# Performance work log

Measured on AMD Instinct MI355X. Metric: run time of the kernel, lower is better.

The kernel has to match this reference:

```python
import jax, jax.numpy as jnp
import numpy as np

BN_EPS = 1e-5
N_NODES = 131072
C_IN = 32
C_OUT = 32
K = 27  # 3x3x3 kernel taps


def setup_inputs() -> dict:
    key = jax.random.key(0)
    k1, k2, k3 = jax.random.split(key, 3)
    data_in = jax.random.normal(k1, (1, C_IN, N_NODES, 1), dtype=jnp.float32)
    neigh = jax.random.randint(k2, (N_NODES, K), 0, N_NODES, dtype=jnp.int32)
    weight = jax.random.normal(k3, (K * C_IN, C_OUT), dtype=jnp.float32) * (1.0 / np.sqrt(K * C_IN))
    gamma = jnp.ones((C_OUT,), dtype=jnp.float32)
    beta = jnp.zeros((C_OUT,), dtype=jnp.float32)
    return {"data_in": data_in, "neigh": neigh, "weight": weight, "gamma": gamma, "beta": beta}


def reference(data_in, neigh, weight, gamma, beta):
    # data_in: [1, C_in, N, 1] -> node-major features [N, C_in]
    x = jnp.transpose(data_in[0, :, :, 0])  # [N, C_in]
    # Octree sparse conv: gather 27-neighborhood per node, then matmul.
    g = x[neigh]                              # [N, K, C_in] irregular gather
    g = g.reshape(g.shape[0], K * C_IN)       # [N, K*C_in]
    out = g @ weight                          # [N, C_out]
    # BatchNorm2d over [1, C_out, N, 1]: per-channel stats over the N nodes (training mode, biased var)
    mean = jnp.mean(out, axis=0)
    var = jnp.mean(jnp.square(out - mean), axis=0)
    out = (out - mean) * jax.lax.rsqrt(var + BN_EPS) * gamma + beta
    # ReLU
    out = jnp.maximum(out, 0.0)
    # back to O-CNN layout [1, C_out, N, 1]
    return jnp.transpose(out)[None, :, :, None]
```

## Files before the change

kernel.cpp:

```cpp
#include <hip/hip_runtime.h>

#define N_NODES 131072
#define C_IN 32
#define C_OUT 32
#define KTAPS 27
#define BN_EPS 1e-5f

typedef __bf16 bf16x8 __attribute__((ext_vector_type(8)));
typedef float  f32x4  __attribute__((ext_vector_type(4)));


static __device__ __forceinline__ unsigned short f2bf(float f) {
    unsigned int u = __float_as_uint(f);
    unsigned int r = (u + 0x7FFFu + ((u >> 16) & 1u)) >> 16;
    return (unsigned short)r;
}

__global__ __launch_bounds__(256) void k_prep_x(const float* __restrict__ in,
                                                unsigned short* __restrict__ xb) {
    const int n = blockIdx.x * 256 + threadIdx.x;
    unsigned short v[C_IN];
#pragma unroll
    for (int c = 0; c < C_IN; ++c) v[c] = f2bf(in[(size_t)c * N_NODES + n]);
    uint4* dst = reinterpret_cast<uint4*>(xb + (size_t)n * C_IN);
#pragma unroll
    for (int q = 0; q < 4; ++q) {
        uint4 pk;
        pk.x = (unsigned)v[q * 8 + 0] | ((unsigned)v[q * 8 + 1] << 16);
        pk.y = (unsigned)v[q * 8 + 2] | ((unsigned)v[q * 8 + 3] << 16);
        pk.z = (unsigned)v[q * 8 + 4] | ((unsigned)v[q * 8 + 5] << 16);
        pk.w = (unsigned)v[q * 8 + 6] | ((unsigned)v[q * 8 + 7] << 16);
        dst[q] = pk;
    }
}

__global__ __launch_bounds__(256) void k_prep_w(const float* __restrict__ w,
                                                unsigned short* __restrict__ wlay) {
    const int g = blockIdx.x * 256 + threadIdx.x;
    if (g >= KTAPS * 2 * 64) return;
    const int k = g >> 7;
    const int rem = g & 127;
    const int h = rem >> 6;
    const int l = rem & 63;
    unsigned short v[8];
#pragma unroll
    for (int j = 0; j < 8; ++j) {
        const int c  = ((l >> 4) << 3) + j;
        const int co = (h << 4) + (l & 15);
        v[j] = f2bf(w[(size_t)(k * C_IN + c) * C_OUT + co]);
    }
    uint4 pk;
    pk.x = (unsigned)v[0] | ((unsigned)v[1] << 16);
    pk.y = (unsigned)v[2] | ((unsigned)v[3] << 16);
    pk.z = (unsigned)v[4] | ((unsigned)v[5] << 16);
    pk.w = (unsigned)v[6] | ((unsigned)v[7] << 16);
    *reinterpret_cast<uint4*>(wlay + (size_t)g * 8) = pk;
}

__global__ __launch_bounds__(256) void k_conv_mfma(const unsigned short* __restrict__ xb,
                                                   const int* __restrict__ neigh,
                                                   const unsigned short* __restrict__ wlay,
                                                   float* __restrict__ out) {
    const int wid  = threadIdx.x >> 6;
    const int lane = threadIdx.x & 63;
    const int lr   = lane & 15;
    const int lg   = lane >> 4;
    const int nb   = (blockIdx.x * 4 + wid) * 16;

    const int* nrow = neigh + (size_t)(nb + lr) * KTAPS;
    int nidx[KTAPS];
#pragma unroll
    for (int k = 0; k < KTAPS; ++k) nidx[k] = nrow[k];

    f32x4 acc0 = {0.f, 0.f, 0.f, 0.f};
    f32x4 acc1 = {0.f, 0.f, 0.f, 0.f};

#pragma unroll
    for (int k = 0; k < KTAPS; ++k) {
        const bf16x8 xf = *reinterpret_cast<const bf16x8*>(xb + (size_t)nidx[k] * C_IN + lg * 8);
        const bf16x8 w0 = *reinterpret_cast<const bf16x8*>(wlay + ((size_t)(k * 2 + 0) * 64 + lane) * 8);
        const bf16x8 w1 = *reinterpret_cast<const bf16x8*>(wlay + ((size_t)(k * 2 + 1) * 64 + lane) * 8);
        acc0 = __builtin_amdgcn_mfma_f32_16x16x32_bf16(w0, xf, acc0, 0, 0, 0);
        acc1 = __builtin_amdgcn_mfma_f32_16x16x32_bf16(w1, xf, acc1, 0, 0, 0);
    }

#pragma unroll
    for (int r = 0; r < 4; ++r) {
        out[(size_t)(lg * 4 + r) * N_NODES + nb + lr]        = acc0[r];
        out[(size_t)(16 + lg * 4 + r) * N_NODES + nb + lr]   = acc1[r];
    }
}

__global__ __launch_bounds__(256) void k_stats(const float* __restrict__ out,
                                               float* __restrict__ sums) {
    const int c     = blockIdx.x >> 3;
    const int chunk = blockIdx.x & 7;
    const float4* base = reinterpret_cast<const float4*>(out + (size_t)c * N_NODES + chunk * (N_NODES / 8));
    float s = 0.f, s2 = 0.f;
    for (int i = threadIdx.x; i < N_NODES / 8 / 4; i += 256) {
        float4 v = base[i];
        s  += v.x + v.y + v.z + v.w;
        s2 += v.x * v.x + v.y * v.y + v.z * v.z + v.w * v.w;
    }
#pragma unroll
    for (int off = 32; off >= 1; off >>= 1) {
        s  += __shfl_xor(s,  off);
        s2 += __shfl_xor(s2, off);
    }
    __shared__ float ls[8];
    const int wid = threadIdx.x >> 6;
    if ((threadIdx.x & 63) == 0) { ls[wid * 2] = s; ls[wid * 2 + 1] = s2; }
    __syncthreads();
    if (threadIdx.x == 0) {
        float ts  = ls[0] + ls[2] + ls[4] + ls[6];
        float ts2 = ls[1] + ls[3] + ls[5] + ls[7];
        atomicAdd(&sums[c], ts);
        atomicAdd(&sums[C_OUT + c], ts2);
    }
}

__global__ __launch_bounds__(256) void k_bnrelu(float* __restrict__ out,
                                                const float* __restrict__ sums,
                                                const float* __restrict__ gamma,
                                                const float* __restrict__ beta) {
    const size_t gid = (size_t)blockIdx.x * 256 + threadIdx.x;
    const int co = (int)(gid / (N_NODES / 4));
    const float inv_n = 1.0f / (float)N_NODES;
    const float mean = sums[co] * inv_n;
    const float var  = sums[C_OUT + co] * inv_n - mean * mean;
    const float scale = rsqrtf(var + BN_EPS) * gamma[co];
    const float bias  = beta[co] - mean * scale;

    float4* p = reinterpret_cast<float4*>(out);
    float4 v = p[gid];
    v.x = fmaxf(fmaf(v.x, scale, bias), 0.0f);
    v.y = fmaxf(fmaf(v.y, scale, bias), 0.0f);
    v.z = fmaxf(fmaf(v.z, scale, bias), 0.0f);
    v.w = fmaxf(fmaf(v.w, scale, bias), 0.0f);
    p[gid] = v;
}

extern "C" void kernel_launch(void* const* d_in, const int* in_sizes, int n_in,
                              void* d_out, int out_size, void* d_ws, size_t ws_size,
                              hipStream_t stream) {
    const float* data_in = (const float*)d_in[0];
    const int*   neigh   = (const int*)d_in[1];
    const float* weight  = (const float*)d_in[2];
    const float* gamma   = (const float*)d_in[3];
    const float* beta    = (const float*)d_in[4];
    float* out = (float*)d_out;

    unsigned short* xb   = (unsigned short*)d_ws;
    unsigned short* wlay = xb + (size_t)N_NODES * C_IN;
    float* sums = (float*)(wlay + (size_t)KTAPS * 2 * 64 * 8);

    hipMemsetAsync(sums, 0, 2 * C_OUT * sizeof(float), stream);
    k_prep_x<<<N_NODES / 256, 256, 0, stream>>>(data_in, xb);
    k_prep_w<<<(KTAPS * 2 * 64 + 255) / 256, 256, 0, stream>>>(weight, wlay);
    k_conv_mfma<<<N_NODES / 64, 256, 0, stream>>>(xb, neigh, wlay, out);
    k_stats<<<C_OUT * 8, 256, 0, stream>>>(out, sums);
    k_bnrelu<<<(N_NODES * C_OUT / 4) / 256, 256, 0, stream>>>(out, sums, gamma, beta);
}
```

Before: 82.52 us.

## Partition gather by source range in passes, stage weights in LDS, merge prep kernels

The conv kernel now makes three passes over the node index range. Each pass only gathers neighbors whose index falls in the current third and redirects the rest to a zero padding row, to improve cache locality of the irregular gather. Weights are staged in shared memory, each wave processes 64 nodes instead of 16, and the two prep kernels are merged into one launch. The cost is triple the MFMA and index-load work, plus fewer blocks and waves to hide gather latency.

Result: slower. 125.0 us (+51.5%).

```diff
diff --git a/kernel.cpp b/kernel.cpp
--- a/kernel.cpp
+++ b/kernel.cpp
@@ -5,6 +5,7 @@
 #define C_OUT 32
 #define KTAPS 27
 #define BN_EPS 1e-5f
+#define NPASS 3
 
 typedef __bf16 bf16x8 __attribute__((ext_vector_type(8)));
 typedef float  f32x4  __attribute__((ext_vector_type(4)));
@@ -16,8 +17,10 @@
     return (unsigned short)r;
 }
 
-__global__ __launch_bounds__(256) void k_prep_x(const float* __restrict__ in,
-                                                unsigned short* __restrict__ xb) {
+__global__ __launch_bounds__(256) void k_prep(const float* __restrict__ in,
+                                              const float* __restrict__ w,
+                                              unsigned short* __restrict__ xb,
+                                              unsigned short* __restrict__ wlay) {
     const int n = blockIdx.x * 256 + threadIdx.x;
     unsigned short v[C_IN];
 #pragma unroll
@@ -32,63 +35,84 @@
         pk.w = (unsigned)v[q * 8 + 6] | ((unsigned)v[q * 8 + 7] << 16);
         dst[q] = pk;
     }
+    if (blockIdx.x == 0) {
+        if (threadIdx.x < 4) {
+            uint4 z = {0u, 0u, 0u, 0u};
+            reinterpret_cast<uint4*>(xb + (size_t)N_NODES * C_IN)[threadIdx.x] = z;
+        }
+        for (int g = threadIdx.x; g < KTAPS * 2 * 64; g += 256) {
+            const int k = g >> 7;
+            const int rem = g & 127;
+            const int h = rem >> 6;
+            const int l = rem & 63;
+            unsigned short wv[8];
+#pragma unroll
+            for (int j = 0; j < 8; ++j) {
+                const int c  = ((l >> 4) << 3) + j;
+                const int co = (h << 4) + (l & 15);
+                wv[j] = f2bf(w[(size_t)(k * C_IN + c) * C_OUT + co]);
+            }
+            uint4 pk;
+            pk.x = (unsigned)wv[0] | ((unsigned)wv[1] << 16);
+            pk.y = (unsigned)wv[2] | ((unsigned)wv[3] << 16);
+            pk.z = (unsigned)wv[4] | ((unsigned)wv[5] << 16);
+            pk.w = (unsigned)wv[6] | ((unsigned)wv[7] << 16);
+            *reinterpret_cast<uint4*>(wlay + (size_t)g * 8) = pk;
+        }
+    }
 }
 
-__global__ __launch_bounds__(256) void k_prep_w(const float* __restrict__ w,
-                                                unsigned short* __restrict__ wlay) {
-    const int g = blockIdx.x * 256 + threadIdx.x;
-    if (g >= KTAPS * 2 * 64) return;
-    const int k = g >> 7;
-    const int rem = g & 127;
-    const int h = rem >> 6;
-    const int l = rem & 63;
-    unsigned short v[8];
-#pragma unroll
-    for (int j = 0; j < 8; ++j) {
-        const int c  = ((l >> 4) << 3) + j;
-        const int co = (h << 4) + (l & 15);
-        v[j] = f2bf(w[(size_t)(k * C_IN + c) * C_OUT + co]);
+__global__ __launch_bounds__(256, 2) void k_conv_mfma(const unsigned short* __restrict__ xb,
+                                                      const int* __restrict__ neigh,
+                                                      const unsigned short* __restrict__ wlay,
+                                                      float* __restrict__ out) {
+    __shared__ unsigned short wl[KTAPS * 2 * 64 * 8];
+
+    {
+        const uint4* src = reinterpret_cast<const uint4*>(wlay);
+        uint4* d = reinterpret_cast<uint4*>(wl);
+        for (int i = threadIdx.x; i < KTAPS * 2 * 64; i += 256) d[i] = src[i];
     }
-    uint4 pk;
-    pk.x = (unsigned)v[0] | ((unsigned)v[1] << 16);
-    pk.y = (unsigned)v[2] | ((unsigned)v[3] << 16);
-    pk.z = (unsigned)v[4] | ((unsigned)v[5] << 16);
-    pk.w = (unsigned)v[6] | ((unsigned)v[7] << 16);
-    *reinterpret_cast<uint4*>(wlay + (size_t)g * 8) = pk;
-}
+    __syncthreads();
 
-__global__ __launch_bounds__(256) void k_conv_mfma(const unsigned short* __restrict__ xb,
-                                                   const int* __restrict__ neigh,
-                                                   const unsigned short* __restrict__ wlay,
-                                                   float* __restrict__ out) {
     const int wid  = threadIdx.x >> 6;
     const int lane = threadIdx.x & 63;
     const int lr   = lane & 15;
     const int lg   = lane >> 4;
-    const int nb   = (blockIdx.x * 4 + wid) * 16;
+    const int nb   = blockIdx.x * 256 + wid * 64;
 
-    const int* nrow = neigh + (size_t)(nb + lr) * KTAPS;
-    int nidx[KTAPS];
+    f32x4 acc[4][2];
 #pragma unroll
-    for (int k = 0; k < KTAPS; ++k) nidx[k] = nrow[k];
+    for (int g = 0; g < 4; ++g) {
+        acc[g][0] = (f32x4){0.f, 0.f, 0.f, 0.f};
+        acc[g][1] = (f32x4){0.f, 0.f, 0.f, 0.f};
+    }
 
-    f32x4 acc0 = {0.f, 0.f, 0.f, 0.f};
-    f32x4 acc1 = {0.f, 0.f, 0.f, 0.f};
-
+    for (int p = 0; p < NPASS; ++p) {
+        const int lo = (p * N_NODES) / NPASS;
+        const int hi = ((p + 1) * N_NODES) / NPASS;
+        for (int k = 0; k < KTAPS; ++k) {
+            const bf16x8 w0 = *reinterpret_cast<const bf16x8*>(wl + ((size_t)(k * 2 + 0) * 64 + lane) * 8);
+            const bf16x8 w1 = *reinterpret_cast<const bf16x8*>(wl + ((size_t)(k * 2 + 1) * 64 + lane) * 8);
 #pragma unroll
-    for (int k = 0; k < KTAPS; ++k) {
-        const bf16x8 xf = *reinterpret_cast<const bf16x8*>(xb + (size_t)nidx[k] * C_IN + lg * 8);
-        const bf16x8 w0 = *reinterpret_cast<const bf16x8*>(wlay + ((size_t)(k * 2 + 0) * 64 + lane) * 8);
-        const bf16x8 w1 = *reinterpret_cast<const bf16x8*>(wlay + ((size_t)(k * 2 + 1) * 64 + lane) * 8);
-        acc0 = __builtin_amdgcn_mfma_f32_16x16x32_bf16(w0, xf, acc0, 0, 0, 0);
-        acc1 = __builtin_amdgcn_mfma_f32_16x16x32_bf16(w1, xf, acc1, 0, 0, 0);
+            for (int g = 0; g < 4; ++g) {
+                const int idx = neigh[(size_t)(nb + g * 16 + lr) * KTAPS + k];
+                const bool valid = (idx >= lo) && (idx < hi);
+                const int src = valid ? idx : N_NODES;
+                const bf16x8 xf = *reinterpret_cast<const bf16x8*>(xb + (size_t)src * C_IN + lg * 8);
+                acc[g][0] = __builtin_amdgcn_mfma_f32_16x16x32_bf16(w0, xf, acc[g][0], 0, 0, 0);
+                acc[g][1] = __builtin_amdgcn_mfma_f32_16x16x32_bf16(w1, xf, acc[g][1], 0, 0, 0);
+            }
+        }
     }
 
 #pragma unroll
-    for (int r = 0; r < 4; ++r) {
-        out[(size_t)(lg * 4 + r) * N_NODES + nb + lr]        = acc0[r];
-        out[(size_t)(16 + lg * 4 + r) * N_NODES + nb + lr]   = acc1[r];
-    }
+    for (int g = 0; g < 4; ++g)
+#pragma unroll
+        for (int r = 0; r < 4; ++r) {
+            out[(size_t)(lg * 4 + r) * N_NODES + nb + g * 16 + lr]      = acc[g][0][r];
+            out[(size_t)(16 + lg * 4 + r) * N_NODES + nb + g * 16 + lr] = acc[g][1][r];
+        }
 }
 
 __global__ __launch_bounds__(256) void k_stats(const float* __restrict__ out,
@@ -151,13 +175,12 @@
     float* out = (float*)d_out;
 
     unsigned short* xb   = (unsigned short*)d_ws;
-    unsigned short* wlay = xb + (size_t)N_NODES * C_IN;
+    unsigned short* wlay = xb + (size_t)(N_NODES + 1) * C_IN;
     float* sums = (float*)(wlay + (size_t)KTAPS * 2 * 64 * 8);
 
     hipMemsetAsync(sums, 0, 2 * C_OUT * sizeof(float), stream);
-    k_prep_x<<<N_NODES / 256, 256, 0, stream>>>(data_in, xb);
-    k_prep_w<<<(KTAPS * 2 * 64 + 255) / 256, 256, 0, stream>>>(weight, wlay);
-    k_conv_mfma<<<N_NODES / 64, 256, 0, stream>>>(xb, neigh, wlay, out);
+    k_prep<<<N_NODES / 256, 256, 0, stream>>>(data_in, weight, xb, wlay);
+    k_conv_mfma<<<N_NODES / 256, 256, 0, stream>>>(xb, neigh, wlay, out);
     k_stats<<<C_OUT * 8, 256, 0, stream>>>(out, sums);
     k_bnrelu<<<(N_NODES * C_OUT / 4) / 256, 256, 0, stream>>>(out, sums, gamma, beta);
 }
```
